# Kernel optimization log

Hardware: AMD Instinct MI355X
Metric: run time of the kernel (lower is better)

## Reference

```python
import jax, jax.numpy as jnp
import numpy as np

B, T, I, H = 64, 512, 1024, 1024


def _xavier(key, shape):
    fan_in, fan_out = shape[0], shape[1]
    a = jnp.sqrt(6.0 / (fan_in + fan_out))
    return jax.random.uniform(key, shape, jnp.float32, -a, a)


def setup_inputs() -> dict:
    key = jax.random.key(0)
    ks = jax.random.split(key, 9)
    inp = {"x": jax.random.normal(ks[0], (B, T, I), jnp.float32)}
    names = [("W_ii", (I, H)), ("W_hi", (H, H)), ("W_if", (I, H)), ("W_hf", (H, H)),
             ("W_ig", (I, H)), ("W_hg", (H, H)), ("W_io", (I, H)), ("W_ho", (H, H))]
    for k, (name, shape) in zip(ks[1:], names):
        inp[name] = _xavier(k, shape)
    for name in ["b_ii", "b_hi", "b_if", "b_hf", "b_ig", "b_hg", "b_io", "b_ho"]:
        inp[name] = jnp.zeros((H,), jnp.float32)
    return inp


def _lstm(x, W_ii, W_hi, b_ii, b_hi, W_if, W_hf, b_if, b_hf,
          W_ig, W_hg, b_ig, b_hg, W_io, W_ho, b_io, b_ho):
    # Fuse the 4 input-projection GEMMs into one [I, 4H] matmul over all timesteps,
    # and the 4 recurrent GEMMs into one [H, 4H] matmul per step. Math is identical.
    Wx = jnp.concatenate([W_ii, W_if, W_ig, W_io], axis=1)   # [I, 4H]
    Wh = jnp.concatenate([W_hi, W_hf, W_hg, W_ho], axis=1)   # [H, 4H]
    b = jnp.concatenate([b_ii + b_hi, b_if + b_hf, b_ig + b_hg, b_io + b_ho])  # [4H]
    bsz = x.shape[0]
    Hd = W_hi.shape[0]
    xg = jnp.einsum('bti,ig->btg', x, Wx) + b                # [B, T, 4H]
    xg = jnp.swapaxes(xg, 0, 1)                              # [T, B, 4H]

    def step(carry, xg_t):
        h, c = carry
        g = xg_t + h @ Wh                                    # [B, 4H]
        i_t = jax.nn.sigmoid(g[:, 0 * Hd:1 * Hd])
        f_t = jax.nn.sigmoid(g[:, 1 * Hd:2 * Hd])
        g_t = jnp.tanh(g[:, 2 * Hd:3 * Hd])
        o_t = jax.nn.sigmoid(g[:, 3 * Hd:4 * Hd])
        c = f_t * c + i_t * g_t
        h = o_t * jnp.tanh(c)
        return (h, c), None

    h0 = jnp.zeros((bsz, Hd), x.dtype)
    c0 = jnp.zeros((bsz, Hd), x.dtype)
    (h_t, c_t), _ = jax.lax.scan(step, (h0, c0), xg)
    return h_t, c_t


def reference(x, W_ii, W_hi, b_ii, b_hi, W_if, W_hf, b_if, b_hf,
              W_ig, W_hg, b_ig, b_hg, W_io, W_ho, b_io, b_ho):
    return _lstm(x, W_ii, W_hi, b_ii, b_hi, W_if, W_hf, b_if, b_hf,
                 W_ig, W_hg, b_ig, b_hg, W_io, W_ho, b_io, b_ho)
```

## Files before the change

kernel.cpp:

```cpp
#include <hip/hip_runtime.h>
#include <cstdint>
#include <cstddef>
#include <string.h>

typedef __bf16 bf16;
typedef bf16 bf16x4 __attribute__((ext_vector_type(4)));
typedef bf16 bf16x8 __attribute__((ext_vector_type(8)));
typedef float f32x4 __attribute__((ext_vector_type(4)));
typedef unsigned long long u64;

#define B_   64
#define T_   512
#define I_   1024
#define H_   1024
#define BT_  32768
#define NBL  64
#define NJ   16

#define WS_XBF   ((size_t)0)
#define WS_WXP   ((size_t)67108864)
#define WS_WHP   ((size_t)75497472)
#define WS_XG    ((size_t)83886080)
#define WS_HB    ((size_t)352321536)
#define WS_ARR   ((size_t)352583680)
#define WS_NEED  ((size_t)352600064)

#define GLD_LDS16(gptr, lptr) \
  __builtin_amdgcn_global_load_lds((const __attribute__((address_space(1))) void*)(gptr), \
                                   (__attribute__((address_space(3))) void*)(lptr), 16, 0, 0)

__device__ __forceinline__ float sigmoidf_(float x) { return 1.0f / (1.0f + __expf(-x)); }
__device__ __forceinline__ float tanhf_(float x) { float e = __expf(2.0f * x); return 1.0f - 2.0f / (e + 1.0f); }
__device__ __forceinline__ float lo2f(unsigned u) { unsigned v = u << 16; float f; memcpy(&f, &v, 4); return f; }
__device__ __forceinline__ float hi2f(unsigned u) { unsigned v = u & 0xffff0000u; float f; memcpy(&f, &v, 4); return f; }
__device__ __forceinline__ unsigned short b2s(bf16 h) { unsigned short s; memcpy(&s, &h, 2); return s; }


__global__ __launch_bounds__(256) void k_cvt_x(const float4* __restrict__ in,
                                               bf16* __restrict__ out, int n4) {
  int i = blockIdx.x * blockDim.x + threadIdx.x;
  int stride = gridDim.x * blockDim.x;
  for (; i < n4; i += stride) {
    float4 v = in[i];
    bf16x4 r = { (bf16)v.x, (bf16)v.y, (bf16)v.z, (bf16)v.w };
    *(bf16x4*)(out + (size_t)i * 4) = r;
  }
}

__global__ __launch_bounds__(256) void k_pack_wx(const float* __restrict__ W,
                                                 bf16* __restrict__ wxp, int gate) {
  __shared__ bf16 tile[32][33];
  int bx = blockIdx.x & 31, by = blockIdx.x >> 5;
  int tx = threadIdx.x & 31, ty = threadIdx.x >> 5;
  int k0 = by * 32, n0 = bx * 32;
  for (int r = 0; r < 32; r += 8)
    tile[ty + r][tx] = (bf16)W[(size_t)(k0 + ty + r) * H_ + n0 + tx];
  __syncthreads();
  for (int r = 0; r < 32; r += 8)
    wxp[(size_t)(gate * H_ + n0 + ty + r) * I_ + k0 + tx] = tile[tx][ty + r];
}

__global__ __launch_bounds__(256) void k_pack_wh(const float* __restrict__ W,
                                                 bf16* __restrict__ whp, int gate) {
  __shared__ bf16 tile[32][33];
  int bx = blockIdx.x & 31, by = blockIdx.x >> 5;
  int tx = threadIdx.x & 31, ty = threadIdx.x >> 5;
  int k0 = by * 32, u0 = bx * 32;
  for (int r = 0; r < 32; r += 8)
    tile[ty + r][tx] = (bf16)W[(size_t)(k0 + ty + r) * H_ + u0 + tx];
  __syncthreads();
  for (int r = 0; r < 32; r += 8) {
    int u = u0 + ty + r;
    int k = k0 + tx;
    size_t addr = ((size_t)(u >> 4) * 128 + (k >> 3)) * 512 +
                  (size_t)(gate * 16 + (u & 15)) * 8 + (k & 7);
    whp[addr] = tile[tx][ty + r];
  }
}

__global__ __launch_bounds__(256) void k_gemm_xg(const bf16* __restrict__ A,
                                                 const bf16* __restrict__ Bt,
                                                 bf16* __restrict__ xg) {
  __shared__ bf16 As[128 * 64];
  __shared__ bf16 Bs[128 * 64];
  int bid = blockIdx.x;
  int bm = bid >> 5, bn = bid & 31;
  int m0 = bm * 128, n0 = bn * 128;
  int tid = threadIdx.x, lane = tid & 63, w = tid >> 6;
  int lr = lane & 15, lk = lane >> 4;
  int sr = lane >> 3, sk = (lane & 7) * 8;
  int wm = (w >> 1) * 64, wn = (w & 1) * 64;
  f32x4 acc[4][4] = {};

  for (int k0 = 0; k0 < 1024; k0 += 64) {
    __syncthreads();
    for (int i = 0; i < 4; ++i) {
      int idx = w * 4 + i;
      const bf16* ga = A + (size_t)(m0 + idx * 8 + sr) * 1024 + k0 + sk;
      GLD_LDS16(ga, &As[idx * 512]);
      const bf16* gb = Bt + (size_t)(n0 + idx * 8 + sr) * 1024 + k0 + sk;
      GLD_LDS16(gb, &Bs[idx * 512]);
    }
    asm volatile("s_waitcnt vmcnt(0)" ::: "memory");
    __syncthreads();
#pragma unroll
    for (int kk = 0; kk < 64; kk += 32) {
      bf16x8 af[4], bfr[4];
#pragma unroll
      for (int i = 0; i < 4; ++i)
        af[i] = *(const bf16x8*)&As[(wm + i * 16 + lr) * 64 + kk + lk * 8];
#pragma unroll
      for (int j = 0; j < 4; ++j)
        bfr[j] = *(const bf16x8*)&Bs[(wn + j * 16 + lr) * 64 + kk + lk * 8];
#pragma unroll
      for (int i = 0; i < 4; ++i)
#pragma unroll
        for (int j = 0; j < 4; ++j)
          acc[i][j] = __builtin_amdgcn_mfma_f32_16x16x32_bf16(af[i], bfr[j], acc[i][j], 0, 0, 0);
    }
  }
#pragma unroll
  for (int i = 0; i < 4; ++i) {
#pragma unroll
    for (int j = 0; j < 4; ++j) {
      int n = n0 + wn + j * 16 + lr;
      int u = n & 1023, g = n >> 10;
      int blk = u >> 4, c = g * 16 + (u & 15);
      int mb = m0 + wm + i * 16 + lk * 4;
#pragma unroll
      for (int r = 0; r < 4; ++r) {
        int m = mb + r;
        int t = m & 511, bb = m >> 9;
        xg[(((size_t)t * NBL + blk) * B_ + bb) * 64 + c] = (bf16)acc[i][j][r];
      }
    }
  }
}

__global__ __launch_bounds__(512) void k_lstm(const bf16* __restrict__ xg,
                                              const bf16* __restrict__ whp,
                                              bf16* hb,
                                              float* __restrict__ out,
                                              unsigned* arr,
                                              const float* __restrict__ bii, const float* __restrict__ bhi,
                                              const float* __restrict__ bif, const float* __restrict__ bhf,
                                              const float* __restrict__ big, const float* __restrict__ bhg,
                                              const float* __restrict__ bio, const float* __restrict__ bho) {
  __shared__ bf16 whl[65536];
  __shared__ float gl[64 * 65];
  int blk = blockIdx.x;
  int tid = threadIdx.x;
  int lane = tid & 63, w = tid >> 6;
  int lr = lane & 15, lk = lane >> 4;
  int wm = (w >> 1) * 16;
  int kh = w & 1;

  {
    const bf16* src = whp + (size_t)blk * 65536;
#pragma unroll
    for (int i = 0; i < 16; ++i)
      *(bf16x8*)&whl[(size_t)(i * 512 + tid) * 8] = *(const bf16x8*)&src[(size_t)(i * 512 + tid) * 8];
  }

  int eu2 = tid & 7, b = tid >> 3;
  int u0g = blk * NJ + eu2 * 2, u1g = u0g + 1;
  float bi0 = bii[u0g] + bhi[u0g], bi1 = bii[u1g] + bhi[u1g];
  float bf0 = bif[u0g] + bhf[u0g], bf1 = bif[u1g] + bhf[u1g];
  float bg0 = big[u0g] + bhg[u0g], bg1 = big[u1g] + bhg[u1g];
  float bo0 = bio[u0g] + bho[u0g], bo1 = bio[u1g] + bho[u1g];
  float c0 = 0.f, c1 = 0.f;

  const char* hb_c = (const char*)hb;
  __syncthreads();

  for (int t = 0; t < T_; ++t) {
    if (t > 0) {
      unsigned v;
      do {
        v = __hip_atomic_load(arr + (kh * 32 + (lane & 31)) * 32,
                              __ATOMIC_RELAXED, __HIP_MEMORY_SCOPE_AGENT);
      } while (!__all((int)(v >= (unsigned)t)));
      __builtin_amdgcn_sched_barrier(0);
    }

    bf16x8 af[16];
    const char* hbase = hb_c + (size_t)(t & 1) * 131072 + (size_t)(wm + lr) * 2048 +
                        (size_t)kh * 1024 + (size_t)lk * 16;
#pragma unroll
    for (int i = 0; i < 16; ++i)
      asm volatile("global_load_dwordx4 %0, %1, off sc0 sc1"
                   : "=v"(af[i]) : "v"(hbase + (size_t)i * 64));

    unsigned xv[4];
    const char* xgb = (const char*)xg + (((size_t)t * NBL + blk) * B_ + b) * 128 + eu2 * 4;
#pragma unroll
    for (int g = 0; g < 4; ++g)
      asm volatile("global_load_dword %0, %1, off"
                   : "=v"(xv[g]) : "v"(xgb + (size_t)g * 32));

    f32x4 acc[4] = {};
#define MFMA_GRP(G)                                                                   \
    _Pragma("unroll")                                                                 \
    for (int ii = 0; ii < 4; ++ii) {                                                  \
      int i = (G) * 4 + ii;                                                           \
      int kg = kh * 64 + i * 4 + lk;                                                  \
      _Pragma("unroll")                                                               \
      for (int nt = 0; nt < 4; ++nt) {                                                \
        bf16x8 bb = *(const bf16x8*)&whl[(kg * 64 + nt * 16 + lr) * 8];               \
        acc[nt] = __builtin_amdgcn_mfma_f32_16x16x32_bf16(af[i], bb, acc[nt], 0, 0, 0); \
      }                                                                               \
    }
    asm volatile("s_waitcnt vmcnt(16)" ::: "memory");
    __builtin_amdgcn_sched_barrier(0);
    MFMA_GRP(0)
    asm volatile("s_waitcnt vmcnt(12)" ::: "memory");
    __builtin_amdgcn_sched_barrier(0);
    MFMA_GRP(1)
    asm volatile("s_waitcnt vmcnt(8)" ::: "memory");
    __builtin_amdgcn_sched_barrier(0);
    MFMA_GRP(2)
    asm volatile("s_waitcnt vmcnt(4)" ::: "memory");
    __builtin_amdgcn_sched_barrier(0);
    MFMA_GRP(3)
#undef MFMA_GRP

    int grow = wm + lk * 4;
    if (kh == 0) {
#pragma unroll
      for (int nt = 0; nt < 4; ++nt)
#pragma unroll
        for (int r = 0; r < 4; ++r)
          gl[(grow + r) * 65 + nt * 16 + lr] = acc[nt][r];
    }
    __syncthreads();
    if (kh == 1) {
#pragma unroll
      for (int nt = 0; nt < 4; ++nt)
#pragma unroll
        for (int r = 0; r < 4; ++r)
          gl[(grow + r) * 65 + nt * 16 + lr] += acc[nt][r];
    }
    __syncthreads();

    asm volatile("s_waitcnt vmcnt(0)" ::: "memory");
    __builtin_amdgcn_sched_barrier(0);
    int gb = b * 65 + eu2 * 2;
    float gi0 = gl[gb]          + lo2f(xv[0]) + bi0;
    float gi1 = gl[gb + 1]      + hi2f(xv[0]) + bi1;
    float gf0 = gl[gb + 16]     + lo2f(xv[1]) + bf0;
    float gf1 = gl[gb + 17]     + hi2f(xv[1]) + bf1;
    float gg0 = gl[gb + 32]     + lo2f(xv[2]) + bg0;
    float gg1 = gl[gb + 33]     + hi2f(xv[2]) + bg1;
    float go0 = gl[gb + 48]     + lo2f(xv[3]) + bo0;
    float go1 = gl[gb + 49]     + hi2f(xv[3]) + bo1;
    c0 = sigmoidf_(gf0) * c0 + sigmoidf_(gi0) * tanhf_(gg0);
    c1 = sigmoidf_(gf1) * c1 + sigmoidf_(gi1) * tanhf_(gg1);
    float hv0 = sigmoidf_(go0) * tanhf_(c0);
    float hv1 = sigmoidf_(go1) * tanhf_(c1);

    if (t == T_ - 1) {
      out[(size_t)b * H_ + u0g] = hv0;
      out[(size_t)b * H_ + u1g] = hv1;
      out[(size_t)B_ * H_ + b * H_ + u0g] = c0;
      out[(size_t)B_ * H_ + b * H_ + u1g] = c1;
      break;
    }

    unsigned hp = (unsigned)b2s((bf16)hv0) | ((unsigned)b2s((bf16)hv1) << 16);
    unsigned* hw = (unsigned*)(hb + (size_t)((t + 1) & 1) * (B_ * H_));
    __hip_atomic_store(hw + b * 512 + blk * 8 + eu2, hp, __ATOMIC_RELAXED, __HIP_MEMORY_SCOPE_AGENT);

    asm volatile("s_waitcnt vmcnt(0)" ::: "memory");
    __syncthreads();
    if (tid == 0)
      __hip_atomic_store(arr + blk * 32, (unsigned)(t + 1), __ATOMIC_RELAXED, __HIP_MEMORY_SCOPE_AGENT);
  }
}


extern "C" void kernel_launch(void* const* d_in, const int* in_sizes, int n_in,
                              void* d_out, int out_size, void* d_ws, size_t ws_size,
                              hipStream_t stream) {
  if (ws_size < WS_NEED) return;

  const float* x = (const float*)d_in[0];
  const float* W_ii = (const float*)d_in[1];
  const float* W_hi = (const float*)d_in[2];
  const float* W_if = (const float*)d_in[3];
  const float* W_hf = (const float*)d_in[4];
  const float* W_ig = (const float*)d_in[5];
  const float* W_hg = (const float*)d_in[6];
  const float* W_io = (const float*)d_in[7];
  const float* W_ho = (const float*)d_in[8];
  const float* b_ii = (const float*)d_in[9];
  const float* b_hi = (const float*)d_in[10];
  const float* b_if = (const float*)d_in[11];
  const float* b_hf = (const float*)d_in[12];
  const float* b_ig = (const float*)d_in[13];
  const float* b_hg = (const float*)d_in[14];
  const float* b_io = (const float*)d_in[15];
  const float* b_ho = (const float*)d_in[16];

  char* ws = (char*)d_ws;
  bf16* xbf = (bf16*)(ws + WS_XBF);
  bf16* wxp = (bf16*)(ws + WS_WXP);
  bf16* whp = (bf16*)(ws + WS_WHP);
  bf16* xgp = (bf16*)(ws + WS_XG);
  bf16* hbp = (bf16*)(ws + WS_HB);
  unsigned* arrp = (unsigned*)(ws + WS_ARR);
  float* outp = (float*)d_out;

  hipMemsetAsync(ws + WS_HB, 0, 262144 + 8192, stream);

  k_cvt_x<<<2048, 256, 0, stream>>>((const float4*)x, xbf, BT_ * I_ / 4);
  const float* wx_g[4] = {W_ii, W_if, W_ig, W_io};
  const float* wh_g[4] = {W_hi, W_hf, W_hg, W_ho};
  for (int g = 0; g < 4; ++g) {
    k_pack_wx<<<1024, 256, 0, stream>>>(wx_g[g], wxp, g);
    k_pack_wh<<<1024, 256, 0, stream>>>(wh_g[g], whp, g);
  }

  k_gemm_xg<<<dim3(256 * 32), 256, 0, stream>>>(xbf, wxp, xgp);

  void* args[] = {
      (void*)&xgp, (void*)&whp, (void*)&hbp, (void*)&outp, (void*)&arrp,
      (void*)&b_ii, (void*)&b_hi, (void*)&b_if, (void*)&b_hf,
      (void*)&b_ig, (void*)&b_hg, (void*)&b_io, (void*)&b_ho};
  hipLaunchCooperativeKernel((const void*)k_lstm, dim3(NBL), dim3(512), args, 0, stream);
}
```

Before: 4.007 ms.

## Remove per-step block barriers with per-wave gate-interleaved LSTM and fine-grained flags

Reorders the packed recurrent weights and the xg layout so the four gates of each hidden unit sit next to each other. Each wave then computes the full K reduction for its batch rows and two unit tiles, and a quad shuffle-transpose hands each lane all four gates. This drops the LDS gate buffer and both __syncthreads per timestep. Synchronisation becomes per-row-group flags written by individual waves, so consumers wait only on the row slices they need. The costs are more h loads per wave (32 instead of 16), scattered 2-byte stores, and a capped spin loop that could exit before the data is ready.

```diff
diff --git a/kernel.cpp b/kernel.cpp
--- a/kernel.cpp
+++ b/kernel.cpp
@@ -34,6 +34,29 @@
 __device__ __forceinline__ float lo2f(unsigned u) { unsigned v = u << 16; float f; memcpy(&f, &v, 4); return f; }
 __device__ __forceinline__ float hi2f(unsigned u) { unsigned v = u & 0xffff0000u; float f; memcpy(&f, &v, 4); return f; }
 __device__ __forceinline__ unsigned short b2s(bf16 h) { unsigned short s; memcpy(&s, &h, 2); return s; }
+
+__device__ __forceinline__ f32x4 quad_transpose(f32x4 v, int lane) {
+  f32x4 m1, m2;
+  float s10 = __shfl_xor(v[1], 1);
+  float s11 = __shfl_xor(v[0], 1);
+  float s12 = __shfl_xor(v[3], 1);
+  float s13 = __shfl_xor(v[2], 1);
+  bool e1 = (lane & 1) == 0;
+  m1[0] = e1 ? v[0] : s10;
+  m1[1] = e1 ? s11 : v[1];
+  m1[2] = e1 ? v[2] : s12;
+  m1[3] = e1 ? s13 : v[3];
+  float s20 = __shfl_xor(m1[2], 2);
+  float s21 = __shfl_xor(m1[3], 2);
+  float s22 = __shfl_xor(m1[0], 2);
+  float s23 = __shfl_xor(m1[1], 2);
+  bool e2 = (lane & 2) == 0;
+  m2[0] = e2 ? m1[0] : s20;
+  m2[1] = e2 ? m1[1] : s21;
+  m2[2] = e2 ? s22 : m1[2];
+  m2[3] = e2 ? s23 : m1[3];
+  return m2;
+}
 
 
 __global__ __launch_bounds__(256) void k_cvt_x(const float4* __restrict__ in,
@@ -73,7 +96,7 @@
     int u = u0 + ty + r;
     int k = k0 + tx;
     size_t addr = ((size_t)(u >> 4) * 128 + (k >> 3)) * 512 +
-                  (size_t)(gate * 16 + (u & 15)) * 8 + (k & 7);
+                  (size_t)((u & 15) * 4 + gate) * 8 + (k & 7);
     whp[addr] = tile[tx][ty + r];
   }
 }
@@ -125,7 +148,7 @@
     for (int j = 0; j < 4; ++j) {
       int n = n0 + wn + j * 16 + lr;
       int u = n & 1023, g = n >> 10;
-      int blk = u >> 4, c = g * 16 + (u & 15);
+      int blk = u >> 4, c = (u & 15) * 4 + g;
       int mb = m0 + wm + i * 16 + lk * 4;
 #pragma unroll
       for (int r = 0; r < 4; ++r) {
@@ -147,13 +170,11 @@
                                               const float* __restrict__ big, const float* __restrict__ bhg,
                                               const float* __restrict__ bio, const float* __restrict__ bho) {
   __shared__ bf16 whl[65536];
-  __shared__ float gl[64 * 65];
   int blk = blockIdx.x;
   int tid = threadIdx.x;
   int lane = tid & 63, w = tid >> 6;
+  int r16 = w >> 1, nh = w & 1;
   int lr = lane & 15, lk = lane >> 4;
-  int wm = (w >> 1) * 16;
-  int kh = w & 1;
 
   {
     const bf16* src = whp + (size_t)blk * 65536;
@@ -162,118 +183,115 @@
       *(bf16x8*)&whl[(size_t)(i * 512 + tid) * 8] = *(const bf16x8*)&src[(size_t)(i * 512 + tid) * 8];
   }
 
-  int eu2 = tid & 7, b = tid >> 3;
-  int u0g = blk * NJ + eu2 * 2, u1g = u0g + 1;
-  float bi0 = bii[u0g] + bhi[u0g], bi1 = bii[u1g] + bhi[u1g];
-  float bf0 = bif[u0g] + bhf[u0g], bf1 = bif[u1g] + bhf[u1g];
-  float bg0 = big[u0g] + bhg[u0g], bg1 = big[u1g] + bhg[u1g];
-  float bo0 = bio[u0g] + bho[u0g], bo1 = bio[u1g] + bho[u1g];
-  float c0 = 0.f, c1 = 0.f;
+  int prow = (lane >> 4) * 4 + (lane & 3);
+  int grow = r16 * 16 + prow;
+  int ul0 = (nh * 2 + 0) * 4 + ((lane & 15) >> 2);
+  int ul1 = (nh * 2 + 1) * 4 + ((lane & 15) >> 2);
+  int ug0 = blk * NJ + ul0, ug1 = blk * NJ + ul1;
+  f32x4 bias0 = { bii[ug0] + bhi[ug0], bif[ug0] + bhf[ug0],
+                  big[ug0] + bhg[ug0], bio[ug0] + bho[ug0] };
+  f32x4 bias1 = { bii[ug1] + bhi[ug1], bif[ug1] + bhf[ug1],
+                  big[ug1] + bhg[ug1], bio[ug1] + bho[ug1] };
+  float cs0 = 0.f, cs1 = 0.f;
 
   const char* hb_c = (const char*)hb;
+  const char* flg = (const char*)arr;
   __syncthreads();
 
   for (int t = 0; t < T_; ++t) {
     if (t > 0) {
-      unsigned v;
+      const char* fp = flg + ((size_t)r16 * 64 + lane) * 8;
+      u64 fv; int cap = 0;
+      bool ok;
       do {
-        v = __hip_atomic_load(arr + (kh * 32 + (lane & 31)) * 32,
-                              __ATOMIC_RELAXED, __HIP_MEMORY_SCOPE_AGENT);
-      } while (!__all((int)(v >= (unsigned)t)));
+        asm volatile("global_load_dwordx2 %0, %1, off sc0 sc1\n\ts_waitcnt vmcnt(0)"
+                     : "=v"(fv) : "v"(fp) : "memory");
+        unsigned f0 = (unsigned)fv, f1 = (unsigned)(fv >> 32);
+        ok = (f0 >= (unsigned)t) && (f1 >= (unsigned)t);
+      } while (!__all((int)ok) && ++cap < 300000);
       __builtin_amdgcn_sched_barrier(0);
     }
 
-    bf16x8 af[16];
-    const char* hbase = hb_c + (size_t)(t & 1) * 131072 + (size_t)(wm + lr) * 2048 +
-                        (size_t)kh * 1024 + (size_t)lk * 16;
-#pragma unroll
-    for (int i = 0; i < 16; ++i)
+    bf16x8 af[32];
+    const char* hbase = hb_c + (size_t)(t & 1) * 131072 +
+                        (size_t)(r16 * 16 + lr) * 2048 + (size_t)lk * 16;
+#pragma unroll
+    for (int i = 0; i < 32; ++i)
       asm volatile("global_load_dwordx4 %0, %1, off sc0 sc1"
                    : "=v"(af[i]) : "v"(hbase + (size_t)i * 64));
-
-    unsigned xv[4];
-    const char* xgb = (const char*)xg + (((size_t)t * NBL + blk) * B_ + b) * 128 + eu2 * 4;
-#pragma unroll
-    for (int g = 0; g < 4; ++g)
-      asm volatile("global_load_dword %0, %1, off"
-                   : "=v"(xv[g]) : "v"(xgb + (size_t)g * 32));
-
-    f32x4 acc[4] = {};
-#define MFMA_GRP(G)                                                                   \
-    _Pragma("unroll")                                                                 \
-    for (int ii = 0; ii < 4; ++ii) {                                                  \
-      int i = (G) * 4 + ii;                                                           \
-      int kg = kh * 64 + i * 4 + lk;                                                  \
-      _Pragma("unroll")                                                               \
-      for (int nt = 0; nt < 4; ++nt) {                                                \
-        bf16x8 bb = *(const bf16x8*)&whl[(kg * 64 + nt * 16 + lr) * 8];               \
-        acc[nt] = __builtin_amdgcn_mfma_f32_16x16x32_bf16(af[i], bb, acc[nt], 0, 0, 0); \
-      }                                                                               \
-    }
-    asm volatile("s_waitcnt vmcnt(16)" ::: "memory");
+    u64 xq0, xq1;
+    {
+      const char* xb = (const char*)xg + ((((size_t)t * NBL + blk) * B_ + grow) * 64) * 2;
+      asm volatile("global_load_dwordx2 %0, %1, off" : "=v"(xq0) : "v"(xb + ul0 * 8));
+      asm volatile("global_load_dwordx2 %0, %1, off" : "=v"(xq1) : "v"(xb + ul1 * 8));
+    }
+
+    f32x4 acc0 = {}, acc1 = {};
+#define MFMA_GRP(G)                                                                     \
+    _Pragma("unroll")                                                                   \
+    for (int ii = 0; ii < 8; ++ii) {                                                    \
+      int i = (G) * 8 + ii;                                                             \
+      bf16x8 b0 = *(const bf16x8*)&whl[((i * 4 + lk) * 64 + (nh * 2 + 0) * 16 + lr) * 8]; \
+      bf16x8 b1 = *(const bf16x8*)&whl[((i * 4 + lk) * 64 + (nh * 2 + 1) * 16 + lr) * 8]; \
+      acc0 = __builtin_amdgcn_mfma_f32_16x16x32_bf16(af[i], b0, acc0, 0, 0, 0);         \
+      acc1 = __builtin_amdgcn_mfma_f32_16x16x32_bf16(af[i], b1, acc1, 0, 0, 0);         \
+    }
+    asm volatile("s_waitcnt vmcnt(26)" ::: "memory");
     __builtin_amdgcn_sched_barrier(0);
     MFMA_GRP(0)
-    asm volatile("s_waitcnt vmcnt(12)" ::: "memory");
+    asm volatile("s_waitcnt vmcnt(18)" ::: "memory");
     __builtin_amdgcn_sched_barrier(0);
     MFMA_GRP(1)
-    asm volatile("s_waitcnt vmcnt(8)" ::: "memory");
+    asm volatile("s_waitcnt vmcnt(10)" ::: "memory");
     __builtin_amdgcn_sched_barrier(0);
     MFMA_GRP(2)
-    asm volatile("s_waitcnt vmcnt(4)" ::: "memory");
+    asm volatile("s_waitcnt vmcnt(2)" ::: "memory");
     __builtin_amdgcn_sched_barrier(0);
     MFMA_GRP(3)
 #undef MFMA_GRP
-
-    int grow = wm + lk * 4;
-    if (kh == 0) {
-#pragma unroll
-      for (int nt = 0; nt < 4; ++nt)
-#pragma unroll
-        for (int r = 0; r < 4; ++r)
-          gl[(grow + r) * 65 + nt * 16 + lr] = acc[nt][r];
-    }
-    __syncthreads();
-    if (kh == 1) {
-#pragma unroll
-      for (int nt = 0; nt < 4; ++nt)
-#pragma unroll
-        for (int r = 0; r < 4; ++r)
-          gl[(grow + r) * 65 + nt * 16 + lr] += acc[nt][r];
-    }
-    __syncthreads();
-
     asm volatile("s_waitcnt vmcnt(0)" ::: "memory");
     __builtin_amdgcn_sched_barrier(0);
-    int gb = b * 65 + eu2 * 2;
-    float gi0 = gl[gb]          + lo2f(xv[0]) + bi0;
-    float gi1 = gl[gb + 1]      + hi2f(xv[0]) + bi1;
-    float gf0 = gl[gb + 16]     + lo2f(xv[1]) + bf0;
-    float gf1 = gl[gb + 17]     + hi2f(xv[1]) + bf1;
-    float gg0 = gl[gb + 32]     + lo2f(xv[2]) + bg0;
-    float gg1 = gl[gb + 33]     + hi2f(xv[2]) + bg1;
-    float go0 = gl[gb + 48]     + lo2f(xv[3]) + bo0;
-    float go1 = gl[gb + 49]     + hi2f(xv[3]) + bo1;
-    c0 = sigmoidf_(gf0) * c0 + sigmoidf_(gi0) * tanhf_(gg0);
-    c1 = sigmoidf_(gf1) * c1 + sigmoidf_(gi1) * tanhf_(gg1);
-    float hv0 = sigmoidf_(go0) * tanhf_(c0);
-    float hv1 = sigmoidf_(go1) * tanhf_(c1);
+
+    f32x4 g0 = quad_transpose(acc0, lane);
+    f32x4 g1 = quad_transpose(acc1, lane);
+
+    unsigned x0l = (unsigned)xq0, x0h = (unsigned)(xq0 >> 32);
+    unsigned x1l = (unsigned)xq1, x1h = (unsigned)(xq1 >> 32);
+    float gi0 = g0[0] + lo2f(x0l) + bias0[0];
+    float gf0 = g0[1] + hi2f(x0l) + bias0[1];
+    float gg0 = g0[2] + lo2f(x0h) + bias0[2];
+    float go0 = g0[3] + hi2f(x0h) + bias0[3];
+    float gi1 = g1[0] + lo2f(x1l) + bias1[0];
+    float gf1 = g1[1] + hi2f(x1l) + bias1[1];
+    float gg1 = g1[2] + lo2f(x1h) + bias1[2];
+    float go1 = g1[3] + hi2f(x1h) + bias1[3];
+    cs0 = sigmoidf_(gf0) * cs0 + sigmoidf_(gi0) * tanhf_(gg0);
+    cs1 = sigmoidf_(gf1) * cs1 + sigmoidf_(gi1) * tanhf_(gg1);
+    float hv0 = sigmoidf_(go0) * tanhf_(cs0);
+    float hv1 = sigmoidf_(go1) * tanhf_(cs1);
 
     if (t == T_ - 1) {
-      out[(size_t)b * H_ + u0g] = hv0;
-      out[(size_t)b * H_ + u1g] = hv1;
-      out[(size_t)B_ * H_ + b * H_ + u0g] = c0;
-      out[(size_t)B_ * H_ + b * H_ + u1g] = c1;
+      out[(size_t)grow * H_ + ug0] = hv0;
+      out[(size_t)grow * H_ + ug1] = hv1;
+      out[(size_t)B_ * H_ + (size_t)grow * H_ + ug0] = cs0;
+      out[(size_t)B_ * H_ + (size_t)grow * H_ + ug1] = cs1;
       break;
     }
 
-    unsigned hp = (unsigned)b2s((bf16)hv0) | ((unsigned)b2s((bf16)hv1) << 16);
-    unsigned* hw = (unsigned*)(hb + (size_t)((t + 1) & 1) * (B_ * H_));
-    __hip_atomic_store(hw + b * 512 + blk * 8 + eu2, hp, __ATOMIC_RELAXED, __HIP_MEMORY_SCOPE_AGENT);
+    {
+      unsigned hb0 = (unsigned)b2s((bf16)hv0);
+      unsigned hb1 = (unsigned)b2s((bf16)hv1);
+      const char* hn = hb_c + (size_t)((t + 1) & 1) * 131072 + (size_t)grow * 2048;
+      asm volatile("global_store_short %0, %1, off sc0 sc1" :: "v"(hn + ug0 * 2), "v"(hb0) : "memory");
+      asm volatile("global_store_short %0, %1, off sc0 sc1" :: "v"(hn + ug1 * 2), "v"(hb1) : "memory");
+    }
 
     asm volatile("s_waitcnt vmcnt(0)" ::: "memory");
-    __syncthreads();
-    if (tid == 0)
-      __hip_atomic_store(arr + blk * 32, (unsigned)(t + 1), __ATOMIC_RELAXED, __HIP_MEMORY_SCOPE_AGENT);
+    if (lane == 0) {
+      unsigned tv = (unsigned)(t + 1);
+      const char* fa = flg + ((size_t)r16 * 64 + blk) * 8 + nh * 4;
+      asm volatile("global_store_dword %0, %1, off sc0 sc1" :: "v"(fa), "v"(tv) : "memory");
+    }
   }
 }
 
```

After: 7.740 ms. 93.2% more time.

## Drop split-K LDS reduction in LSTM recurrence and use per-row-group flags

Applied to the files above, without the earlier changes.

The recurrent kernel goes from 512 to 256 threads. Each wave now computes the full K=1024 dot product for its 16 batch rows, which removes the LDS gate buffer and two __syncthreads per step. The xg layout is interleaved so each lane reads its four gates with one 8-byte load, and gate math is done directly from the MFMA accumulators. Synchronisation becomes per-wave flags (one per row group and block) written after each wave's h stores, so waves only wait on the matching row group of other blocks. The cost is twice the h loads and MFMA chain per wave, and a bounded spin cap that could in principle exit early.

```diff
diff --git a/kernel.cpp b/kernel.cpp
--- a/kernel.cpp
+++ b/kernel.cpp
@@ -17,7 +17,7 @@
 #define NBL  64
 #define NJ   16
 
-#define WS_XBF   ((size_t)0)
+#define WS_XBF   ((size_t)0              )
 #define WS_WXP   ((size_t)67108864)
 #define WS_WHP   ((size_t)75497472)
 #define WS_XG    ((size_t)83886080)
@@ -125,7 +125,7 @@
     for (int j = 0; j < 4; ++j) {
       int n = n0 + wn + j * 16 + lr;
       int u = n & 1023, g = n >> 10;
-      int blk = u >> 4, c = g * 16 + (u & 15);
+      int blk = u >> 4, c = (u & 15) * 4 + g;
       int mb = m0 + wm + i * 16 + lk * 4;
 #pragma unroll
       for (int r = 0; r < 4; ++r) {
@@ -137,7 +137,7 @@
   }
 }
 
-__global__ __launch_bounds__(512) void k_lstm(const bf16* __restrict__ xg,
+__global__ __launch_bounds__(256) void k_lstm(const bf16* __restrict__ xg,
                                               const bf16* __restrict__ whp,
                                               bf16* hb,
                                               float* __restrict__ out,
@@ -147,133 +147,119 @@
                                               const float* __restrict__ big, const float* __restrict__ bhg,
                                               const float* __restrict__ bio, const float* __restrict__ bho) {
   __shared__ bf16 whl[65536];
-  __shared__ float gl[64 * 65];
   int blk = blockIdx.x;
   int tid = threadIdx.x;
-  int lane = tid & 63, w = tid >> 6;
+  int lane = tid & 63, rg = tid >> 6;
   int lr = lane & 15, lk = lane >> 4;
-  int wm = (w >> 1) * 16;
-  int kh = w & 1;
 
   {
     const bf16* src = whp + (size_t)blk * 65536;
 #pragma unroll
-    for (int i = 0; i < 16; ++i)
-      *(bf16x8*)&whl[(size_t)(i * 512 + tid) * 8] = *(const bf16x8*)&src[(size_t)(i * 512 + tid) * 8];
-  }
-
-  int eu2 = tid & 7, b = tid >> 3;
-  int u0g = blk * NJ + eu2 * 2, u1g = u0g + 1;
-  float bi0 = bii[u0g] + bhi[u0g], bi1 = bii[u1g] + bhi[u1g];
-  float bf0 = bif[u0g] + bhf[u0g], bf1 = bif[u1g] + bhf[u1g];
-  float bg0 = big[u0g] + bhg[u0g], bg1 = big[u1g] + bhg[u1g];
-  float bo0 = bio[u0g] + bho[u0g], bo1 = bio[u1g] + bho[u1g];
-  float c0 = 0.f, c1 = 0.f;
+    for (int i = 0; i < 32; ++i)
+      *(bf16x8*)&whl[(size_t)(i * 256 + tid) * 8] = *(const bf16x8*)&src[(size_t)(i * 256 + tid) * 8];
+  }
+
+  int ug = blk * NJ + lr;
+  f32x4 bias = { bii[ug] + bhi[ug], bif[ug] + bhf[ug],
+                 big[ug] + bhg[ug], bio[ug] + bho[ug] };
+  float cs[4] = {0.f, 0.f, 0.f, 0.f};
 
   const char* hb_c = (const char*)hb;
+  const char* flg = (const char*)arr;
   __syncthreads();
 
   for (int t = 0; t < T_; ++t) {
     if (t > 0) {
-      unsigned v;
+      const char* fp = flg + ((size_t)rg * 64 + lane) * 4;
+      unsigned fv; int cap = 0;
       do {
-        v = __hip_atomic_load(arr + (kh * 32 + (lane & 31)) * 32,
-                              __ATOMIC_RELAXED, __HIP_MEMORY_SCOPE_AGENT);
-      } while (!__all((int)(v >= (unsigned)t)));
+        asm volatile("global_load_dword %0, %1, off sc0 sc1\n\ts_waitcnt vmcnt(0)"
+                     : "=v"(fv) : "v"(fp) : "memory");
+      } while (!__all((int)(fv >= (unsigned)t)) && ++cap < 300000);
       __builtin_amdgcn_sched_barrier(0);
     }
 
-    bf16x8 af[16];
-    const char* hbase = hb_c + (size_t)(t & 1) * 131072 + (size_t)(wm + lr) * 2048 +
-                        (size_t)kh * 1024 + (size_t)lk * 16;
-#pragma unroll
-    for (int i = 0; i < 16; ++i)
+    bf16x8 af[32];
+    const char* hbase = hb_c + (size_t)(t & 1) * 131072 +
+                        (size_t)(rg * 16 + lr) * 2048 + (size_t)lk * 16;
+#pragma unroll
+    for (int i = 0; i < 32; ++i)
       asm volatile("global_load_dwordx4 %0, %1, off sc0 sc1"
                    : "=v"(af[i]) : "v"(hbase + (size_t)i * 64));
-
-    unsigned xv[4];
-    const char* xgb = (const char*)xg + (((size_t)t * NBL + blk) * B_ + b) * 128 + eu2 * 4;
-#pragma unroll
-    for (int g = 0; g < 4; ++g)
-      asm volatile("global_load_dword %0, %1, off"
-                   : "=v"(xv[g]) : "v"(xgb + (size_t)g * 32));
+    u64 xq[4];
+    {
+      const char* xb = (const char*)xg + (((size_t)t * NBL + blk) * B_ + rg * 16 + lk * 4) * 128 +
+                       (size_t)lr * 8;
+#pragma unroll
+      for (int r = 0; r < 4; ++r)
+        asm volatile("global_load_dwordx2 %0, %1, off" : "=v"(xq[r]) : "v"(xb + (size_t)r * 128));
+    }
 
     f32x4 acc[4] = {};
-#define MFMA_GRP(G)                                                                   \
-    _Pragma("unroll")                                                                 \
-    for (int ii = 0; ii < 4; ++ii) {                                                  \
-      int i = (G) * 4 + ii;                                                           \
-      int kg = kh * 64 + i * 4 + lk;                                                  \
-      _Pragma("unroll")                                                               \
-      for (int nt = 0; nt < 4; ++nt) {                                                \
-        bf16x8 bb = *(const bf16x8*)&whl[(kg * 64 + nt * 16 + lr) * 8];               \
-        acc[nt] = __builtin_amdgcn_mfma_f32_16x16x32_bf16(af[i], bb, acc[nt], 0, 0, 0); \
-      }                                                                               \
-    }
-    asm volatile("s_waitcnt vmcnt(16)" ::: "memory");
+#define MFMA_GRP(G)                                                                        \
+    _Pragma("unroll")                                                                      \
+    for (int ii = 0; ii < 8; ++ii) {                                                       \
+      int i = (G) * 8 + ii;                                                                \
+      _Pragma("unroll")                                                                    \
+      for (int nt = 0; nt < 4; ++nt) {                                                     \
+        bf16x8 bb = *(const bf16x8*)&whl[((i * 4 + lk) * 64 + nt * 16 + lr) * 8];          \
+        acc[nt] = __builtin_amdgcn_mfma_f32_16x16x32_bf16(af[i], bb, acc[nt], 0, 0, 0);    \
+      }                                                                                    \
+    }
+    asm volatile("s_waitcnt vmcnt(28)" ::: "memory");
     __builtin_amdgcn_sched_barrier(0);
     MFMA_GRP(0)
+    asm volatile("s_waitcnt vmcnt(20)" ::: "memory");
+    __builtin_amdgcn_sched_barrier(0);
+    MFMA_GRP(1)
     asm volatile("s_waitcnt vmcnt(12)" ::: "memory");
-    __builtin_amdgcn_sched_barrier(0);
-    MFMA_GRP(1)
-    asm volatile("s_waitcnt vmcnt(8)" ::: "memory");
     __builtin_amdgcn_sched_barrier(0);
     MFMA_GRP(2)
     asm volatile("s_waitcnt vmcnt(4)" ::: "memory");
     __builtin_amdgcn_sched_barrier(0);
     MFMA_GRP(3)
 #undef MFMA_GRP
-
-    int grow = wm + lk * 4;
-    if (kh == 0) {
-#pragma unroll
-      for (int nt = 0; nt < 4; ++nt)
-#pragma unroll
-        for (int r = 0; r < 4; ++r)
-          gl[(grow + r) * 65 + nt * 16 + lr] = acc[nt][r];
-    }
-    __syncthreads();
-    if (kh == 1) {
-#pragma unroll
-      for (int nt = 0; nt < 4; ++nt)
-#pragma unroll
-        for (int r = 0; r < 4; ++r)
-          gl[(grow + r) * 65 + nt * 16 + lr] += acc[nt][r];
-    }
-    __syncthreads();
-
     asm volatile("s_waitcnt vmcnt(0)" ::: "memory");
     __builtin_amdgcn_sched_barrier(0);
-    int gb = b * 65 + eu2 * 2;
-    float gi0 = gl[gb]          + lo2f(xv[0]) + bi0;
-    float gi1 = gl[gb + 1]      + hi2f(xv[0]) + bi1;
-    float gf0 = gl[gb + 16]     + lo2f(xv[1]) + bf0;
-    float gf1 = gl[gb + 17]     + hi2f(xv[1]) + bf1;
-    float gg0 = gl[gb + 32]     + lo2f(xv[2]) + bg0;
-    float gg1 = gl[gb + 33]     + hi2f(xv[2]) + bg1;
-    float go0 = gl[gb + 48]     + lo2f(xv[3]) + bo0;
-    float go1 = gl[gb + 49]     + hi2f(xv[3]) + bo1;
-    c0 = sigmoidf_(gf0) * c0 + sigmoidf_(gi0) * tanhf_(gg0);
-    c1 = sigmoidf_(gf1) * c1 + sigmoidf_(gi1) * tanhf_(gg1);
-    float hv0 = sigmoidf_(go0) * tanhf_(c0);
-    float hv1 = sigmoidf_(go1) * tanhf_(c1);
+
+    float hv[4];
+#pragma unroll
+    for (int r = 0; r < 4; ++r) {
+      unsigned xlo = (unsigned)xq[r], xhi = (unsigned)(xq[r] >> 32);
+      float gi = acc[0][r] + lo2f(xlo) + bias[0];
+      float gf = acc[1][r] + hi2f(xlo) + bias[1];
+      float gg = acc[2][r] + lo2f(xhi) + bias[2];
+      float go = acc[3][r] + hi2f(xhi) + bias[3];
+      cs[r] = sigmoidf_(gf) * cs[r] + sigmoidf_(gi) * tanhf_(gg);
+      hv[r] = sigmoidf_(go) * tanhf_(cs[r]);
+    }
 
     if (t == T_ - 1) {
-      out[(size_t)b * H_ + u0g] = hv0;
-      out[(size_t)b * H_ + u1g] = hv1;
-      out[(size_t)B_ * H_ + b * H_ + u0g] = c0;
-      out[(size_t)B_ * H_ + b * H_ + u1g] = c1;
+#pragma unroll
+      for (int r = 0; r < 4; ++r) {
+        int grow = rg * 16 + lk * 4 + r;
+        out[(size_t)grow * H_ + ug] = hv[r];
+        out[(size_t)B_ * H_ + (size_t)grow * H_ + ug] = cs[r];
+      }
       break;
     }
 
-    unsigned hp = (unsigned)b2s((bf16)hv0) | ((unsigned)b2s((bf16)hv1) << 16);
-    unsigned* hw = (unsigned*)(hb + (size_t)((t + 1) & 1) * (B_ * H_));
-    __hip_atomic_store(hw + b * 512 + blk * 8 + eu2, hp, __ATOMIC_RELAXED, __HIP_MEMORY_SCOPE_AGENT);
+    {
+      const char* hn = hb_c + (size_t)((t + 1) & 1) * 131072;
+#pragma unroll
+      for (int r = 0; r < 4; ++r) {
+        unsigned hbv = (unsigned)b2s((bf16)hv[r]);
+        const char* pa = hn + (size_t)(rg * 16 + lk * 4 + r) * 2048 + (size_t)ug * 2;
+        asm volatile("global_store_short %0, %1, off sc0 sc1" :: "v"(pa), "v"(hbv) : "memory");
+      }
+    }
 
     asm volatile("s_waitcnt vmcnt(0)" ::: "memory");
-    __syncthreads();
-    if (tid == 0)
-      __hip_atomic_store(arr + blk * 32, (unsigned)(t + 1), __ATOMIC_RELAXED, __HIP_MEMORY_SCOPE_AGENT);
+    if (lane == 0) {
+      unsigned tv = (unsigned)(t + 1);
+      const char* fa = flg + ((size_t)rg * 64 + blk) * 4;
+      asm volatile("global_store_dword %0, %1, off sc0 sc1" :: "v"(fa), "v"(tv) : "memory");
+    }
   }
 }
 
@@ -326,5 +312,5 @@
       (void*)&xgp, (void*)&whp, (void*)&hbp, (void*)&outp, (void*)&arrp,
       (void*)&b_ii, (void*)&b_hi, (void*)&b_if, (void*)&b_hf,
       (void*)&b_ig, (void*)&b_hg, (void*)&b_io, (void*)&b_ho};
-  hipLaunchCooperativeKernel((const void*)k_lstm, dim3(NBL), dim3(512), args, 0, stream);
-}
+  hipLaunchCooperativeKernel((const void*)k_lstm, dim3(NBL), dim3(256), args, 0, stream);
+}
```

After: 5.209 ms. +30.0%, slower.

## Replace flag-based step barrier with sentinel-filled per-step hidden-state ring

Applied to the files above, without the earlier changes.

Drops the per-block arrival counters and the spin-wait before each step. Instead, every timestep writes h into its own slice of a 64 MiB ring that is pre-filled with 0xFF, and readers poll the data itself, restarting the load and MFMA sequence whenever a sentinel word is still present. This removes the per-step __syncthreads plus flag store and the separate flag poll from the serial recurrence critical path. In exchange it adds a large memset, reuses the x-bf16 workspace region as the ring, and relies on bf16 pairs never equalling 0xFFFFFFFF (a NaN pattern) and on visibility ordering of the relaxed stores.

```diff
diff --git a/kernel.cpp b/kernel.cpp
--- a/kernel.cpp
+++ b/kernel.cpp
@@ -7,6 +7,7 @@
 typedef bf16 bf16x4 __attribute__((ext_vector_type(4)));
 typedef bf16 bf16x8 __attribute__((ext_vector_type(8)));
 typedef float f32x4 __attribute__((ext_vector_type(4)));
+typedef unsigned u32x4v __attribute__((ext_vector_type(4)));
 typedef unsigned long long u64;
 
 #define B_   64
@@ -22,7 +23,6 @@
 #define WS_WHP   ((size_t)75497472)
 #define WS_XG    ((size_t)83886080)
 #define WS_HB    ((size_t)352321536)
-#define WS_ARR   ((size_t)352583680)
 #define WS_NEED  ((size_t)352600064)
 
 #define GLD_LDS16(gptr, lptr) \
@@ -34,6 +34,17 @@
 __device__ __forceinline__ float lo2f(unsigned u) { unsigned v = u << 16; float f; memcpy(&f, &v, 4); return f; }
 __device__ __forceinline__ float hi2f(unsigned u) { unsigned v = u & 0xffff0000u; float f; memcpy(&f, &v, 4); return f; }
 __device__ __forceinline__ unsigned short b2s(bf16 h) { unsigned short s; memcpy(&s, &h, 2); return s; }
+
+__device__ __forceinline__ bool chk4(const bf16x8* af, int base) {
+  bool ok = true;
+#pragma unroll
+  for (int i = 0; i < 4; ++i) {
+    u32x4v d = __builtin_bit_cast(u32x4v, af[base + i]);
+    ok = ok & (d[0] != 0xFFFFFFFFu) & (d[1] != 0xFFFFFFFFu) &
+         (d[2] != 0xFFFFFFFFu) & (d[3] != 0xFFFFFFFFu);
+  }
+  return ok;
+}
 
 
 __global__ __launch_bounds__(256) void k_cvt_x(const float4* __restrict__ in,
@@ -139,9 +150,9 @@
 
 __global__ __launch_bounds__(512) void k_lstm(const bf16* __restrict__ xg,
                                               const bf16* __restrict__ whp,
-                                              bf16* hb,
+                                              const char* __restrict__ hb0,
+                                              char* ring,
                                               float* __restrict__ out,
-                                              unsigned* arr,
                                               const float* __restrict__ bii, const float* __restrict__ bhi,
                                               const float* __restrict__ bif, const float* __restrict__ bhf,
                                               const float* __restrict__ big, const float* __restrict__ bhg,
@@ -170,59 +181,71 @@
   float bo0 = bio[u0g] + bho[u0g], bo1 = bio[u1g] + bho[u1g];
   float c0 = 0.f, c1 = 0.f;
 
-  const char* hb_c = (const char*)hb;
   __syncthreads();
 
   for (int t = 0; t < T_; ++t) {
-    if (t > 0) {
-      unsigned v;
-      do {
-        v = __hip_atomic_load(arr + (kh * 32 + (lane & 31)) * 32,
-                              __ATOMIC_RELAXED, __HIP_MEMORY_SCOPE_AGENT);
-      } while (!__all((int)(v >= (unsigned)t)));
-      __builtin_amdgcn_sched_barrier(0);
-    }
+    const char* hsrc = (t == 0) ? hb0 : ring + (size_t)(t - 1) * 131072;
+    const char* hbase = hsrc + (size_t)(wm + lr) * 2048 + (size_t)kh * 1024 + (size_t)lk * 16;
+    const char* osec  = hsrc + (size_t)(wm + lr) * 2048 + (size_t)blk * 32 + (size_t)lk * 8;
+    const char* xgb = (const char*)xg + (((size_t)t * NBL + blk) * B_ + b) * 128 + eu2 * 4;
 
     bf16x8 af[16];
-    const char* hbase = hb_c + (size_t)(t & 1) * 131072 + (size_t)(wm + lr) * 2048 +
-                        (size_t)kh * 1024 + (size_t)lk * 16;
+    u64 osv;
+    unsigned xv[4];
+    f32x4 acc[4];
+    int tries = 0;
+    bool ok;
+
+  restart:
+    acc[0] = (f32x4){}; acc[1] = (f32x4){}; acc[2] = (f32x4){}; acc[3] = (f32x4){};
 #pragma unroll
     for (int i = 0; i < 16; ++i)
       asm volatile("global_load_dwordx4 %0, %1, off sc0 sc1"
                    : "=v"(af[i]) : "v"(hbase + (size_t)i * 64));
-
-    unsigned xv[4];
-    const char* xgb = (const char*)xg + (((size_t)t * NBL + blk) * B_ + b) * 128 + eu2 * 4;
+    asm volatile("global_load_dwordx2 %0, %1, off sc0 sc1" : "=v"(osv) : "v"(osec));
 #pragma unroll
     for (int g = 0; g < 4; ++g)
-      asm volatile("global_load_dword %0, %1, off"
-                   : "=v"(xv[g]) : "v"(xgb + (size_t)g * 32));
-
-    f32x4 acc[4] = {};
-#define MFMA_GRP(G)                                                                   \
-    _Pragma("unroll")                                                                 \
-    for (int ii = 0; ii < 4; ++ii) {                                                  \
-      int i = (G) * 4 + ii;                                                           \
-      int kg = kh * 64 + i * 4 + lk;                                                  \
-      _Pragma("unroll")                                                               \
-      for (int nt = 0; nt < 4; ++nt) {                                                \
-        bf16x8 bb = *(const bf16x8*)&whl[(kg * 64 + nt * 16 + lr) * 8];               \
-        acc[nt] = __builtin_amdgcn_mfma_f32_16x16x32_bf16(af[i], bb, acc[nt], 0, 0, 0); \
-      }                                                                               \
-    }
-    asm volatile("s_waitcnt vmcnt(16)" ::: "memory");
-    __builtin_amdgcn_sched_barrier(0);
+      asm volatile("global_load_dword %0, %1, off" : "=v"(xv[g]) : "v"(xgb + (size_t)g * 32));
+
+#define MFMA_GRP(G)                                                                        \
+    _Pragma("unroll")                                                                      \
+    for (int ii = 0; ii < 4; ++ii) {                                                       \
+      int i = (G) * 4 + ii;                                                                \
+      int kg = kh * 64 + i * 4 + lk;                                                       \
+      _Pragma("unroll")                                                                    \
+      for (int nt = 0; nt < 4; ++nt) {                                                     \
+        bf16x8 bb = *(const bf16x8*)&whl[(kg * 64 + nt * 16 + lr) * 8];                    \
+        acc[nt] = __builtin_amdgcn_mfma_f32_16x16x32_bf16(af[i], bb, acc[nt], 0, 0, 0);    \
+      }                                                                                    \
+    }
+    asm volatile("s_waitcnt vmcnt(17)" ::: "memory");
+    __builtin_amdgcn_sched_barrier(0);
+    ok = chk4(af, 0);
+    if (!__all((int)ok)) { asm volatile("s_waitcnt vmcnt(0)" ::: "memory"); if (++tries < 200000) goto restart; }
     MFMA_GRP(0)
-    asm volatile("s_waitcnt vmcnt(12)" ::: "memory");
-    __builtin_amdgcn_sched_barrier(0);
+    asm volatile("s_waitcnt vmcnt(13)" ::: "memory");
+    __builtin_amdgcn_sched_barrier(0);
+    ok = chk4(af, 4);
+    if (!__all((int)ok)) { asm volatile("s_waitcnt vmcnt(0)" ::: "memory"); if (++tries < 200000) goto restart; }
     MFMA_GRP(1)
-    asm volatile("s_waitcnt vmcnt(8)" ::: "memory");
-    __builtin_amdgcn_sched_barrier(0);
+    asm volatile("s_waitcnt vmcnt(9)" ::: "memory");
+    __builtin_amdgcn_sched_barrier(0);
+    ok = chk4(af, 8);
+    if (!__all((int)ok)) { asm volatile("s_waitcnt vmcnt(0)" ::: "memory"); if (++tries < 200000) goto restart; }
     MFMA_GRP(2)
-    asm volatile("s_waitcnt vmcnt(4)" ::: "memory");
-    __builtin_amdgcn_sched_barrier(0);
+    asm volatile("s_waitcnt vmcnt(5)" ::: "memory");
+    __builtin_amdgcn_sched_barrier(0);
+    ok = chk4(af, 12);
+    if (!__all((int)ok)) { asm volatile("s_waitcnt vmcnt(0)" ::: "memory"); if (++tries < 200000) goto restart; }
     MFMA_GRP(3)
 #undef MFMA_GRP
+    asm volatile("s_waitcnt vmcnt(0)" ::: "memory");
+    __builtin_amdgcn_sched_barrier(0);
+    {
+      unsigned o0 = (unsigned)osv, o1 = (unsigned)(osv >> 32);
+      ok = (o0 != 0xFFFFFFFFu) & (o1 != 0xFFFFFFFFu);
+      if (!__all((int)ok)) { if (++tries < 200000) goto restart; }
+    }
 
     int grow = wm + lk * 4;
     if (kh == 0) {
@@ -242,8 +265,6 @@
     }
     __syncthreads();
 
-    asm volatile("s_waitcnt vmcnt(0)" ::: "memory");
-    __builtin_amdgcn_sched_barrier(0);
     int gb = b * 65 + eu2 * 2;
     float gi0 = gl[gb]          + lo2f(xv[0]) + bi0;
     float gi1 = gl[gb + 1]      + hi2f(xv[0]) + bi1;
@@ -267,13 +288,8 @@
     }
 
     unsigned hp = (unsigned)b2s((bf16)hv0) | ((unsigned)b2s((bf16)hv1) << 16);
-    unsigned* hw = (unsigned*)(hb + (size_t)((t + 1) & 1) * (B_ * H_));
+    unsigned* hw = (unsigned*)(ring + (size_t)t * 131072);
     __hip_atomic_store(hw + b * 512 + blk * 8 + eu2, hp, __ATOMIC_RELAXED, __HIP_MEMORY_SCOPE_AGENT);
-
-    asm volatile("s_waitcnt vmcnt(0)" ::: "memory");
-    __syncthreads();
-    if (tid == 0)
-      __hip_atomic_store(arr + blk * 32, (unsigned)(t + 1), __ATOMIC_RELAXED, __HIP_MEMORY_SCOPE_AGENT);
   }
 }
 
@@ -306,11 +322,11 @@
   bf16* wxp = (bf16*)(ws + WS_WXP);
   bf16* whp = (bf16*)(ws + WS_WHP);
   bf16* xgp = (bf16*)(ws + WS_XG);
-  bf16* hbp = (bf16*)(ws + WS_HB);
-  unsigned* arrp = (unsigned*)(ws + WS_ARR);
+  char* hb0 = ws + WS_HB;
+  char* ring = ws + WS_XBF;
   float* outp = (float*)d_out;
 
-  hipMemsetAsync(ws + WS_HB, 0, 262144 + 8192, stream);
+  hipMemsetAsync(hb0, 0, 131072, stream);
 
   k_cvt_x<<<2048, 256, 0, stream>>>((const float4*)x, xbf, BT_ * I_ / 4);
   const float* wx_g[4] = {W_ii, W_if, W_ig, W_io};
@@ -322,8 +338,10 @@
 
   k_gemm_xg<<<dim3(256 * 32), 256, 0, stream>>>(xbf, wxp, xgp);
 
+  hipMemsetAsync(ring, 0xFF, (size_t)512 * 131072, stream);
+
   void* args[] = {
-      (void*)&xgp, (void*)&whp, (void*)&hbp, (void*)&outp, (void*)&arrp,
+      (void*)&xgp, (void*)&whp, (void*)&hb0, (void*)&ring, (void*)&outp,
       (void*)&b_ii, (void*)&b_hi, (void*)&b_if, (void*)&b_hf,
       (void*)&b_ig, (void*)&b_hg, (void*)&b_io, (void*)&b_ho};
   hipLaunchCooperativeKernel((const void*)k_lstm, dim3(NBL), dim3(512), args, 0, stream);
```

After: 5.896 ms. 47.2% more time.
